# Performance work log

Hardware: AMD Instinct MI355X
Metric: run time of the kernel (lower is better)

Reference implementation:

```python
import jax, jax.numpy as jnp
import numpy as np

DIM, DEPTH, MULT = 512, 3, 4
E = 2 ** DEPTH            # 8 experts
HID = MULT * DIM          # 2048
B, S = 4, 1024


def setup_inputs() -> dict:
    key = jax.random.key(0)
    ks = jax.random.split(key, 7)
    sd = 1.0 / np.sqrt(DIM)
    sh = 1.0 / np.sqrt(HID)
    return {
        "x": jax.random.normal(ks[0], (B, S, DIM), dtype=jnp.float32),
        "rw": jax.random.normal(ks[1], (E - 1, DIM), dtype=jnp.float32) * sd,
        "rb": jax.random.normal(ks[2], (E - 1,), dtype=jnp.float32) * sd,
        "w1": jax.random.normal(ks[3], (E, DIM, HID), dtype=jnp.float32) * sd,
        "b1": jax.random.normal(ks[4], (E, HID), dtype=jnp.float32) * sd,
        "w2": jax.random.normal(ks[5], (E, HID, DIM), dtype=jnp.float32) * sh,
        "b2": jax.random.normal(ks[6], (E, DIM), dtype=jnp.float32) * sh,
    }


def _leaf_probs(flat_x, rw, rb):
    # Binary-tree soft routing: level d has 2**d routers at offset 2**d - 1.
    n_tok = flat_x.shape[0]
    leaf = jnp.ones((n_tok, 1), dtype=flat_x.dtype)
    for d in range(DEPTH):
        off, n = 2 ** d - 1, 2 ** d
        logits = flat_x @ rw[off:off + n].T + rb[off:off + n]   # [N, n]
        p = jax.nn.sigmoid(logits)
        # child probs: left = 1-p, right = p
        leaf = (leaf[:, :, None] * jnp.stack([1.0 - p, p], axis=2)).reshape(n_tok, 2 * n)
    return leaf  # [N, E]


def reference(x, rw, rb, w1, b1, w2, b2):
    b, s, dim = x.shape
    flat_x = x.reshape(b * s, dim)                               # [N, D]
    leaf_probs = _leaf_probs(flat_x, rw, rb)                     # [N, E]
    # Dense evaluation of all experts (soft-routing training path).
    h = jnp.einsum('nd,edh->neh', flat_x, w1) + b1[None]         # [N, E, H]
    h = jax.nn.gelu(h, approximate=False)                        # torch nn.GELU (erf)
    y = jnp.einsum('neh,ehd->ned', h, w2) + b2[None]             # [N, E, D]
    out = jnp.einsum('ned,ne->nd', y, leaf_probs)                # [N, D]
    return out.reshape(b, s, dim)
```

## Files before the change

kernel.cpp:

```cpp
#include <hip/hip_runtime.h>
#include <hip/hip_bf16.h>
#include <hip/hip_fp16.h>

#define DIM 512
#define HID 2048
#define NE 8
#define NTOK 4096

typedef _Float16 v8h __attribute__((ext_vector_type(8)));
typedef float v4f __attribute__((ext_vector_type(4)));

__device__ __forceinline__ void load16(const void* g, void* l) {
  __builtin_amdgcn_global_load_lds(
      (const __attribute__((address_space(1))) unsigned int*)g,
      (__attribute__((address_space(3))) unsigned int*)l, 16, 0, 0);
}

__device__ __forceinline__ float gelu_fast(float v) {
  float v2 = v * v;
  float u = v * __builtin_fmaf(0.07135481627f, v2, 1.5957691216f);
  float t = __expf(-u);
  return v * __builtin_amdgcn_rcpf(1.0f + t);
}

__global__ __launch_bounds__(256) void routing_kernel(const float* __restrict__ x,
                                                      const float* __restrict__ rw,
                                                      const float* __restrict__ rb,
                                                      float* __restrict__ leaf,
                                                      _Float16* __restrict__ xh) {
  const int lane = threadIdx.x & 63;
  const int wave = threadIdx.x >> 6;
  const int n = (blockIdx.x << 2) + wave;
  const float4* xv = (const float4*)(x + (size_t)n * DIM);
  const float4 x0 = xv[lane * 2], x1 = xv[lane * 2 + 1];
  v8h o;
  o[0] = (_Float16)x0.x; o[1] = (_Float16)x0.y; o[2] = (_Float16)x0.z; o[3] = (_Float16)x0.w;
  o[4] = (_Float16)x1.x; o[5] = (_Float16)x1.y; o[6] = (_Float16)x1.z; o[7] = (_Float16)x1.w;
  *(v8h*)(xh + (size_t)n * DIM + lane * 8) = o;
  float logits[7];
#pragma unroll
  for (int rr = 0; rr < 7; ++rr) {
    const float4* wv = (const float4*)(rw + rr * DIM);
    const float4 w0 = wv[lane * 2], w1v = wv[lane * 2 + 1];
    float s = x0.x * w0.x + x0.y * w0.y + x0.z * w0.z + x0.w * w0.w +
              x1.x * w1v.x + x1.y * w1v.y + x1.z * w1v.z + x1.w * w1v.w;
#pragma unroll
    for (int o2 = 32; o2; o2 >>= 1) s += __shfl_xor(s, o2, 64);
    logits[rr] = s + rb[rr];
  }
  if (lane < NE) {
    const int eidx = lane;
    const float p0 = 1.f / (1.f + __expf(-logits[0]));
    float f = ((eidx >> 2) & 1) ? p0 : 1.f - p0;
    const float p1 = 1.f / (1.f + __expf(-logits[1 + (eidx >> 2)]));
    f *= ((eidx >> 1) & 1) ? p1 : 1.f - p1;
    const float p2 = 1.f / (1.f + __expf(-logits[3 + (eidx >> 1)]));
    f *= (eidx & 1) ? p2 : 1.f - p2;
    leaf[(size_t)n * NE + eidx] = f;
  }
}

__global__ __launch_bounds__(256) void transpose_cvt2_kernel(const float* __restrict__ w1,
                                                             _Float16* __restrict__ w1t,
                                                             const float* __restrict__ w2,
                                                             _Float16* __restrict__ w2t) {
  int bx = blockIdx.x;
  const float* in;
  _Float16* outp;
  int R, C;
  if (bx < 4096) { in = w1; outp = w1t; R = DIM; C = HID; }
  else { bx -= 4096; in = w2; outp = w2t; R = HID; C = DIM; }
  const int e = bx >> 9;
  const int rem = bx & 511;
  const int tiles_r = R >> 6;
  const int rt = rem % tiles_r;
  const int ct = rem / tiles_r;
  const int r0 = rt << 6, c0 = ct << 5;
  const size_t ebase = (size_t)e * R * C;

  __shared__ float tile[32][65];
  const int tid = threadIdx.x;
#pragma unroll
  for (int it = 0; it < 2; ++it) {
    const int s = tid + (it << 8);
    const int row = s >> 3, cq = s & 7;
    const float4 v = *(const float4*)(in + ebase + (size_t)(r0 + row) * C + c0 + (cq << 2));
    tile[(cq << 2) + 0][row] = v.x;
    tile[(cq << 2) + 1][row] = v.y;
    tile[(cq << 2) + 2][row] = v.z;
    tile[(cq << 2) + 3][row] = v.w;
  }
  __syncthreads();
  const int c = tid >> 3, seg = tid & 7;
  v8h h;
#pragma unroll
  for (int u = 0; u < 8; ++u) h[u] = (_Float16)tile[c][(seg << 3) + u];
  *(v8h*)(outp + ebase + (size_t)(c0 + c) * R + r0 + (seg << 3)) = h;
}

__global__ __launch_bounds__(256) void out_init_kernel(const float* __restrict__ leaf,
                                                       const float* __restrict__ b2,
                                                       float* __restrict__ out) {
  const int g = blockIdx.x * 256 + threadIdx.x;
  const int n = g >> 7, dq = g & 127;
  const float* lp = leaf + (size_t)n * NE;
  float4 acc = {0.f, 0.f, 0.f, 0.f};
#pragma unroll
  for (int e = 0; e < NE; ++e) {
    const float pe = lp[e];
    const float4 bv = *(const float4*)(b2 + (size_t)e * DIM + (dq << 2));
    acc.x += pe * bv.x; acc.y += pe * bv.y; acc.z += pe * bv.z; acc.w += pe * bv.w;
  }
  *(float4*)(out + (size_t)n * DIM + (dq << 2)) = acc;
}

__global__ __launch_bounds__(256) void gemm1_kernel(const _Float16* __restrict__ xh,
                                                    const _Float16* __restrict__ w1t,
                                                    const float* __restrict__ b1,
                                                    const float* __restrict__ leaf,
                                                    _Float16* __restrict__ H) {
  const int bx = blockIdx.x;
  const int e = bx & 7;
  const int t = bx >> 3;
  const int mt = t & 31;
  const int nt = t >> 5;
  const int m0 = mt << 7, n0 = nt << 7;

  __shared__ alignas(16) _Float16 As[128 * 64];
  __shared__ alignas(16) _Float16 Bs[128 * 64];

  const int tid = threadIdx.x;
  const int lane = tid & 63;
  const int wave = tid >> 6;
  const int qm = wave >> 1, qn = wave & 1;
  const int r = lane & 15, q = lane >> 4;

  const _Float16* pa[4];
  const _Float16* pb[4];
  _Float16* la[4];
  _Float16* lb[4];
#pragma unroll
  for (int i = 0; i < 4; ++i) {
    const int ch = (wave << 8) + (i << 6) + lane;
    const int row = ch >> 3;
    const int c8 = (ch & 7) ^ (row & 7);
    pa[i] = xh + (size_t)(m0 + row) * DIM + (c8 << 3);
    pb[i] = w1t + ((size_t)e * HID + n0 + row) * DIM + (c8 << 3);
    la[i] = As + (size_t)ch * 8;
    lb[i] = Bs + (size_t)ch * 8;
  }
  const _Float16* fa[2][4];
  const _Float16* fb[2][4];
#pragma unroll
  for (int ks = 0; ks < 2; ++ks) {
#pragma unroll
    for (int i = 0; i < 4; ++i) {
      const int rowa = (qm << 6) + (i << 4) + r;
      fa[ks][i] = As + (rowa << 6) + ((((ks << 2) + q) ^ (rowa & 7)) << 3);
      const int rowb = (qn << 6) + (i << 4) + r;
      fb[ks][i] = Bs + (rowb << 6) + ((((ks << 2) + q) ^ (rowb & 7)) << 3);
    }
  }

  v4f acc[4][4];
#pragma unroll
  for (int i = 0; i < 4; ++i)
#pragma unroll
    for (int j = 0; j < 4; ++j) acc[i][j] = v4f{0.f, 0.f, 0.f, 0.f};

#pragma unroll
  for (int kk = 0; kk < 8; ++kk) {
#pragma unroll
    for (int i = 0; i < 4; ++i) {
      load16(pa[i] + kk * 64, la[i]);
      load16(pb[i] + kk * 64, lb[i]);
    }
    __syncthreads();
#pragma unroll
    for (int ks = 0; ks < 2; ++ks) {
      v8h a[4], b[4];
#pragma unroll
      for (int i = 0; i < 4; ++i) a[i] = *(const v8h*)fa[ks][i];
#pragma unroll
      for (int j = 0; j < 4; ++j) b[j] = *(const v8h*)fb[ks][j];
#pragma unroll
      for (int i = 0; i < 4; ++i)
#pragma unroll
        for (int j = 0; j < 4; ++j)
          acc[i][j] = __builtin_amdgcn_mfma_f32_16x16x32_f16(a[i], b[j], acc[i][j], 0, 0, 0);
    }
    __syncthreads();
  }

  const float* b1e = b1 + (size_t)e * HID;
  _Float16* He = H + (size_t)e * NTOK * HID;
  float bias[4];
#pragma unroll
  for (int j = 0; j < 4; ++j) bias[j] = b1e[n0 + (qn << 6) + (j << 4) + r];
#pragma unroll
  for (int i = 0; i < 4; ++i) {
    const int rowb = m0 + (qm << 6) + (i << 4) + (q << 2);
#pragma unroll
    for (int rr = 0; rr < 4; ++rr) {
      const int row = rowb + rr;
      const float p = leaf[(size_t)row * NE + e];
      _Float16* hp = He + (size_t)row * HID + n0 + (qn << 6) + r;
#pragma unroll
      for (int j = 0; j < 4; ++j)
        hp[j << 4] = (_Float16)(p * gelu_fast(acc[i][j][rr] + bias[j]));
    }
  }
}

__global__ __launch_bounds__(256) void gemm2_kernel(const _Float16* __restrict__ H,
                                                    const _Float16* __restrict__ w2t,
                                                    float* __restrict__ out) {
  const int bx = blockIdx.x;
  const int e = bx & 7;
  const int mt = (bx >> 3) & 31;
  const int dt = bx >> 8;
  const int m0 = mt << 7, d0 = dt << 7;

  __shared__ alignas(16) _Float16 As[128 * 64];
  __shared__ alignas(16) _Float16 Bs[128 * 64];

  const int tid = threadIdx.x;
  const int lane = tid & 63;
  const int wave = tid >> 6;
  const int qm = wave >> 1, qn = wave & 1;
  const int r = lane & 15, q = lane >> 4;

  const _Float16* pa[4];
  const _Float16* pb[4];
  _Float16* la[4];
  _Float16* lb[4];
#pragma unroll
  for (int i = 0; i < 4; ++i) {
    const int ch = (wave << 8) + (i << 6) + lane;
    const int row = ch >> 3;
    const int c8 = (ch & 7) ^ (row & 7);
    pa[i] = H + ((size_t)e * NTOK + m0 + row) * HID + (c8 << 3);
    pb[i] = w2t + ((size_t)e * DIM + d0 + row) * HID + (c8 << 3);
    la[i] = As + (size_t)ch * 8;
    lb[i] = Bs + (size_t)ch * 8;
  }
  const _Float16* fa[2][4];
  const _Float16* fb[2][4];
#pragma unroll
  for (int ks = 0; ks < 2; ++ks) {
#pragma unroll
    for (int i = 0; i < 4; ++i) {
      const int rowa = (qm << 6) + (i << 4) + r;
      fa[ks][i] = As + (rowa << 6) + ((((ks << 2) + q) ^ (rowa & 7)) << 3);
      const int rowb = (qn << 6) + (i << 4) + r;
      fb[ks][i] = Bs + (rowb << 6) + ((((ks << 2) + q) ^ (rowb & 7)) << 3);
    }
  }

  v4f acc[4][4];
#pragma unroll
  for (int i = 0; i < 4; ++i)
#pragma unroll
    for (int j = 0; j < 4; ++j) acc[i][j] = v4f{0.f, 0.f, 0.f, 0.f};

  for (int ko = 0; ko < 4; ++ko) {
#pragma unroll
    for (int u = 0; u < 8; ++u) {
#pragma unroll
      for (int i = 0; i < 4; ++i) {
        load16(pa[i] + u * 64, la[i]);
        load16(pb[i] + u * 64, lb[i]);
      }
      __syncthreads();
#pragma unroll
      for (int ks = 0; ks < 2; ++ks) {
        v8h a[4], b[4];
#pragma unroll
        for (int i = 0; i < 4; ++i) a[i] = *(const v8h*)fa[ks][i];
#pragma unroll
        for (int j = 0; j < 4; ++j) b[j] = *(const v8h*)fb[ks][j];
#pragma unroll
        for (int i = 0; i < 4; ++i)
#pragma unroll
          for (int j = 0; j < 4; ++j)
            acc[i][j] = __builtin_amdgcn_mfma_f32_16x16x32_f16(a[i], b[j], acc[i][j], 0, 0, 0);
      }
      __syncthreads();
    }
#pragma unroll
    for (int i = 0; i < 4; ++i) { pa[i] += 512; pb[i] += 512; }
  }

#pragma unroll
  for (int i = 0; i < 4; ++i) {
    const int rowb = m0 + (qm << 6) + (i << 4) + (q << 2);
#pragma unroll
    for (int j = 0; j < 4; ++j) {
      const int col = d0 + (qn << 6) + (j << 4) + r;
#pragma unroll
      for (int rr = 0; rr < 4; ++rr)
        atomicAdd(out + (size_t)(rowb + rr) * DIM + col, acc[i][j][rr]);
    }
  }
}

extern "C" void kernel_launch(void* const* d_in, const int* in_sizes, int n_in,
                              void* d_out, int out_size, void* d_ws, size_t ws_size,
                              hipStream_t stream) {
  const float* x  = (const float*)d_in[0];
  const float* rw = (const float*)d_in[1];
  const float* rb = (const float*)d_in[2];
  const float* w1 = (const float*)d_in[3];
  const float* b1 = (const float*)d_in[4];
  const float* w2 = (const float*)d_in[5];
  const float* b2 = (const float*)d_in[6];
  float* out = (float*)d_out;

  char* ws = (char*)d_ws;
  const size_t xh_bytes   = (size_t)NTOK * DIM * 2;
  const size_t w1t_bytes  = (size_t)NE * HID * DIM * 2;
  const size_t w2t_bytes  = (size_t)NE * DIM * HID * 2;
  const size_t leaf_bytes = (size_t)NTOK * NE * 4;
  const size_t H_bytes    = (size_t)NE * NTOK * HID * 2;
  _Float16* xh   = (_Float16*)(ws);
  _Float16* w1t  = (_Float16*)(ws + xh_bytes);
  _Float16* w2t  = (_Float16*)(ws + xh_bytes + w1t_bytes);
  float*    leaf = (float*)(ws + xh_bytes + w1t_bytes + w2t_bytes);
  _Float16* Hbuf = (_Float16*)(ws + xh_bytes + w1t_bytes + w2t_bytes + leaf_bytes);
  if (ws_size < xh_bytes + w1t_bytes + w2t_bytes + leaf_bytes + H_bytes) return;

  routing_kernel<<<1024, 256, 0, stream>>>(x, rw, rb, leaf, xh);
  transpose_cvt2_kernel<<<8192, 256, 0, stream>>>(w1, w1t, w2, w2t);
  out_init_kernel<<<2048, 256, 0, stream>>>(leaf, b2, out);
  gemm1_kernel<<<4096, 256, 0, stream>>>(xh, w1t, b1, leaf, Hbuf);
  gemm2_kernel<<<1024, 256, 0, stream>>>(Hbuf, w2t, out);
}
```

Before: 341.8 us.

## Double-buffer LDS tiles in both GEMMs and fuse output bias init into routing

Both expert GEMM kernels now keep two LDS stages per operand. The loads for the next K-slice are issued right after a single barrier, while MFMAs run on the current slice, which removes the second barrier per step and the exposed global-to-LDS latency. LDS use per block doubles to 64 KB, which may lower the number of resident blocks. Separately, the leaf-probability-weighted b2 bias initialization of the output moves into the routing kernel via shuffles, dropping one kernel launch and the re-read of the leaf buffer.

```diff
diff --git a/kernel.cpp b/kernel.cpp
--- a/kernel.cpp
+++ b/kernel.cpp
@@ -26,8 +26,10 @@
 __global__ __launch_bounds__(256) void routing_kernel(const float* __restrict__ x,
                                                       const float* __restrict__ rw,
                                                       const float* __restrict__ rb,
+                                                      const float* __restrict__ b2,
                                                       float* __restrict__ leaf,
-                                                      _Float16* __restrict__ xh) {
+                                                      _Float16* __restrict__ xh,
+                                                      float* __restrict__ out) {
   const int lane = threadIdx.x & 63;
   const int wave = threadIdx.x >> 6;
   const int n = (blockIdx.x << 2) + wave;
@@ -48,16 +50,27 @@
     for (int o2 = 32; o2; o2 >>= 1) s += __shfl_xor(s, o2, 64);
     logits[rr] = s + rb[rr];
   }
-  if (lane < NE) {
-    const int eidx = lane;
-    const float p0 = 1.f / (1.f + __expf(-logits[0]));
-    float f = ((eidx >> 2) & 1) ? p0 : 1.f - p0;
-    const float p1 = 1.f / (1.f + __expf(-logits[1 + (eidx >> 2)]));
-    f *= ((eidx >> 1) & 1) ? p1 : 1.f - p1;
-    const float p2 = 1.f / (1.f + __expf(-logits[3 + (eidx >> 1)]));
-    f *= (eidx & 1) ? p2 : 1.f - p2;
-    leaf[(size_t)n * NE + eidx] = f;
-  }
+  const int eidx = lane & 7;
+  const float p0 = 1.f / (1.f + __expf(-logits[0]));
+  float f = ((eidx >> 2) & 1) ? p0 : 1.f - p0;
+  const float p1 = 1.f / (1.f + __expf(-logits[1 + (eidx >> 2)]));
+  f *= ((eidx >> 1) & 1) ? p1 : 1.f - p1;
+  const float p2 = 1.f / (1.f + __expf(-logits[3 + (eidx >> 1)]));
+  f *= (eidx & 1) ? p2 : 1.f - p2;
+  if (lane < NE) leaf[(size_t)n * NE + lane] = f;
+  float le[NE];
+#pragma unroll
+  for (int e = 0; e < NE; ++e) le[e] = __shfl(f, e, 64);
+  float4 a0 = {0.f, 0.f, 0.f, 0.f}, a1 = {0.f, 0.f, 0.f, 0.f};
+#pragma unroll
+  for (int e = 0; e < NE; ++e) {
+    const float4* bv = (const float4*)(b2 + (size_t)e * DIM + lane * 8);
+    const float4 u0 = bv[0], u1 = bv[1];
+    a0.x += le[e] * u0.x; a0.y += le[e] * u0.y; a0.z += le[e] * u0.z; a0.w += le[e] * u0.w;
+    a1.x += le[e] * u1.x; a1.y += le[e] * u1.y; a1.z += le[e] * u1.z; a1.w += le[e] * u1.w;
+  }
+  float4* op = (float4*)(out + (size_t)n * DIM + lane * 8);
+  op[0] = a0; op[1] = a1;
 }
 
 __global__ __launch_bounds__(256) void transpose_cvt2_kernel(const float* __restrict__ w1,
@@ -98,22 +111,6 @@
   *(v8h*)(outp + ebase + (size_t)(c0 + c) * R + r0 + (seg << 3)) = h;
 }
 
-__global__ __launch_bounds__(256) void out_init_kernel(const float* __restrict__ leaf,
-                                                       const float* __restrict__ b2,
-                                                       float* __restrict__ out) {
-  const int g = blockIdx.x * 256 + threadIdx.x;
-  const int n = g >> 7, dq = g & 127;
-  const float* lp = leaf + (size_t)n * NE;
-  float4 acc = {0.f, 0.f, 0.f, 0.f};
-#pragma unroll
-  for (int e = 0; e < NE; ++e) {
-    const float pe = lp[e];
-    const float4 bv = *(const float4*)(b2 + (size_t)e * DIM + (dq << 2));
-    acc.x += pe * bv.x; acc.y += pe * bv.y; acc.z += pe * bv.z; acc.w += pe * bv.w;
-  }
-  *(float4*)(out + (size_t)n * DIM + (dq << 2)) = acc;
-}
-
 __global__ __launch_bounds__(256) void gemm1_kernel(const _Float16* __restrict__ xh,
                                                     const _Float16* __restrict__ w1t,
                                                     const float* __restrict__ b1,
@@ -126,8 +123,8 @@
   const int nt = t >> 5;
   const int m0 = mt << 7, n0 = nt << 7;
 
-  __shared__ alignas(16) _Float16 As[128 * 64];
-  __shared__ alignas(16) _Float16 Bs[128 * 64];
+  __shared__ alignas(16) _Float16 As[2 * 8192];
+  __shared__ alignas(16) _Float16 Bs[2 * 8192];
 
   const int tid = threadIdx.x;
   const int lane = tid & 63;
@@ -169,27 +166,33 @@
     for (int j = 0; j < 4; ++j) acc[i][j] = v4f{0.f, 0.f, 0.f, 0.f};
 
 #pragma unroll
+  for (int i = 0; i < 4; ++i) { load16(pa[i], la[i]); load16(pb[i], lb[i]); }
+
+#pragma unroll
   for (int kk = 0; kk < 8; ++kk) {
-#pragma unroll
-    for (int i = 0; i < 4; ++i) {
-      load16(pa[i] + kk * 64, la[i]);
-      load16(pb[i] + kk * 64, lb[i]);
-    }
     __syncthreads();
+    if (kk < 7) {
+      const int off = (((kk + 1) & 1) << 13);
+#pragma unroll
+      for (int i = 0; i < 4; ++i) {
+        load16(pa[i] + (kk + 1) * 64, la[i] + off);
+        load16(pb[i] + (kk + 1) * 64, lb[i] + off);
+      }
+    }
+    const int cp = ((kk & 1) << 13);
 #pragma unroll
     for (int ks = 0; ks < 2; ++ks) {
       v8h a[4], b[4];
 #pragma unroll
-      for (int i = 0; i < 4; ++i) a[i] = *(const v8h*)fa[ks][i];
-#pragma unroll
-      for (int j = 0; j < 4; ++j) b[j] = *(const v8h*)fb[ks][j];
+      for (int i = 0; i < 4; ++i) a[i] = *(const v8h*)(fa[ks][i] + cp);
+#pragma unroll
+      for (int j = 0; j < 4; ++j) b[j] = *(const v8h*)(fb[ks][j] + cp);
 #pragma unroll
       for (int i = 0; i < 4; ++i)
 #pragma unroll
         for (int j = 0; j < 4; ++j)
           acc[i][j] = __builtin_amdgcn_mfma_f32_16x16x32_f16(a[i], b[j], acc[i][j], 0, 0, 0);
     }
-    __syncthreads();
   }
 
   const float* b1e = b1 + (size_t)e * HID;
@@ -221,8 +224,8 @@
   const int dt = bx >> 8;
   const int m0 = mt << 7, d0 = dt << 7;
 
-  __shared__ alignas(16) _Float16 As[128 * 64];
-  __shared__ alignas(16) _Float16 Bs[128 * 64];
+  __shared__ alignas(16) _Float16 As[2 * 8192];
+  __shared__ alignas(16) _Float16 Bs[2 * 8192];
 
   const int tid = threadIdx.x;
   const int lane = tid & 63;
@@ -263,29 +266,35 @@
 #pragma unroll
     for (int j = 0; j < 4; ++j) acc[i][j] = v4f{0.f, 0.f, 0.f, 0.f};
 
+#pragma unroll
+  for (int i = 0; i < 4; ++i) { load16(pa[i], la[i]); load16(pb[i], lb[i]); }
+
   for (int ko = 0; ko < 4; ++ko) {
 #pragma unroll
     for (int u = 0; u < 8; ++u) {
-#pragma unroll
-      for (int i = 0; i < 4; ++i) {
-        load16(pa[i] + u * 64, la[i]);
-        load16(pb[i] + u * 64, lb[i]);
+      __syncthreads();
+      if (!(ko == 3 && u == 7)) {
+        const int off = (((u + 1) & 1) << 13);
+#pragma unroll
+        for (int i = 0; i < 4; ++i) {
+          load16(pa[i] + (u + 1) * 64, la[i] + off);
+          load16(pb[i] + (u + 1) * 64, lb[i] + off);
+        }
       }
-      __syncthreads();
+      const int cp = ((u & 1) << 13);
 #pragma unroll
       for (int ks = 0; ks < 2; ++ks) {
         v8h a[4], b[4];
 #pragma unroll
-        for (int i = 0; i < 4; ++i) a[i] = *(const v8h*)fa[ks][i];
-#pragma unroll
-        for (int j = 0; j < 4; ++j) b[j] = *(const v8h*)fb[ks][j];
+        for (int i = 0; i < 4; ++i) a[i] = *(const v8h*)(fa[ks][i] + cp);
+#pragma unroll
+        for (int j = 0; j < 4; ++j) b[j] = *(const v8h*)(fb[ks][j] + cp);
 #pragma unroll
         for (int i = 0; i < 4; ++i)
 #pragma unroll
           for (int j = 0; j < 4; ++j)
             acc[i][j] = __builtin_amdgcn_mfma_f32_16x16x32_f16(a[i], b[j], acc[i][j], 0, 0, 0);
       }
-      __syncthreads();
     }
 #pragma unroll
     for (int i = 0; i < 4; ++i) { pa[i] += 512; pb[i] += 512; }
@@ -329,9 +338,8 @@
   _Float16* Hbuf = (_Float16*)(ws + xh_bytes + w1t_bytes + w2t_bytes + leaf_bytes);
   if (ws_size < xh_bytes + w1t_bytes + w2t_bytes + leaf_bytes + H_bytes) return;
 
-  routing_kernel<<<1024, 256, 0, stream>>>(x, rw, rb, leaf, xh);
+  routing_kernel<<<1024, 256, 0, stream>>>(x, rw, rb, b2, leaf, xh, out);
   transpose_cvt2_kernel<<<8192, 256, 0, stream>>>(w1, w1t, w2, w2t);
-  out_init_kernel<<<2048, 256, 0, stream>>>(leaf, b2, out);
   gemm1_kernel<<<4096, 256, 0, stream>>>(xh, w1t, b1, leaf, Hbuf);
   gemm2_kernel<<<1024, 256, 0, stream>>>(Hbuf, w2t, out);
 }
```

Result: slower. 359.5 us (+5.2%).
